# Kernel optimization log

Measured on AMD Instinct MI355X. Metric: run time of the kernel, lower is better.

## Reference

```python
import jax, jax.numpy as jnp
import numpy as np

B, C, H, W = 16, 64, 64, 64
K = 512  # n_embeddings


def setup_inputs() -> dict:
    key = jax.random.key(0)
    k1, k2 = jax.random.split(key)
    inputs = jax.random.normal(k1, (B, C, H, W), dtype=jnp.float32)
    emb_weight = jax.random.normal(k2, (K, C), dtype=jnp.float32)
    weight = jnp.ones((K,), dtype=jnp.float32)  # EMA cluster-size buffer
    return {"inputs": inputs, "emb_weight": emb_weight, "weight": weight}


def reference(inputs, emb_weight, weight):
    sg = jax.lax.stop_gradient
    # BCHW -> BHWC
    x = jnp.transpose(inputs, (0, 2, 3, 1))  # [B,H,W,C]
    flat = x.reshape(-1, x.shape[-1])        # [N,C]
    n = flat.shape[0]
    k = emb_weight.shape[0]
    # squared euclidean distances [N,K] (argmin identical to cdist argmin)
    d = (
        jnp.sum(flat * flat, axis=-1, keepdims=True)
        - 2.0 * (flat @ emb_weight.T)
        + jnp.sum(emb_weight * emb_weight, axis=-1)
    )
    indices = jnp.argmin(d, axis=1)  # [N]
    # avg_probs = mean over rows of one-hot mask == normalized histogram
    avg_probs = jnp.bincount(indices, length=k).astype(jnp.float32) / jnp.float32(n)
    perplexity = jnp.exp(-jnp.sum(avg_probs * jnp.log(avg_probs + 1e-10)))
    # straight-through quantization
    q = emb_weight[indices].reshape(x.shape)  # [B,H,W,C]
    quantized = sg(q) + x - sg(x)
    commitment_loss = jnp.mean((sg(quantized) - x) ** 2)
    active_codes = jnp.sum(weight >= 0.01)
    out = jnp.transpose(quantized, (0, 3, 1, 2))  # back to BCHW
    return out, commitment_loss, perplexity, active_codes, indices
```

## Files before the change

kernel.cpp:

```cpp
#include <hip/hip_runtime.h>

#define HW 4096
#define CHW 262144
#define OUT_ELEMS 4194304
#define FLT_BIG 3.4e38f

typedef __attribute__((ext_vector_type(8))) short  short8;
typedef __attribute__((ext_vector_type(4))) float  floatx4;
typedef __attribute__((ext_vector_type(4))) int    intx4;


__device__ __forceinline__ unsigned bf16_rne(float f) {
    unsigned u = __float_as_uint(f);
    return (u + 0x7FFFu + ((u >> 16) & 1u)) >> 16;
}

__device__ __forceinline__ void split8(const float* f, intx4* hi, intx4* lo) {
    unsigned h[4], l[4];
#pragma unroll
    for (int j = 0; j < 4; ++j) {
        const unsigned h0 = bf16_rne(f[2 * j]);
        const unsigned h1 = bf16_rne(f[2 * j + 1]);
        const float hf0 = __uint_as_float(h0 << 16);
        const float hf1 = __uint_as_float(h1 << 16);
        const unsigned l0 = bf16_rne(f[2 * j] - hf0);
        const unsigned l1 = bf16_rne(f[2 * j + 1] - hf1);
        h[j] = h0 | (h1 << 16);
        l[j] = l0 | (l1 << 16);
    }
    *hi = intx4{(int)h[0], (int)h[1], (int)h[2], (int)h[3]};
    *lo = intx4{(int)l[0], (int)l[1], (int)l[2], (int)l[3]};
}

__global__ void vq_prep(const float* __restrict__ emb,
                        unsigned short* __restrict__ pfrag,
                        float* __restrict__ enorm,
                        unsigned* __restrict__ hist,
                        unsigned* __restrict__ done) {
    const int t = threadIdx.x;
    const int lane = t & 63;
    if (blockIdx.x == 0) {
        hist[t] = 0u; hist[t + 256] = 0u;
        if (t == 0) *done = 0u;
    }
    const int code = (blockIdx.x << 2) + (t >> 6);
    const int c = lane;
    const float v = emb[(code << 6) + c];
    const unsigned hb = bf16_rne(v);
    const float hf    = __uint_as_float(hb << 16);
    const unsigned lb = bf16_rne(v - hf);
    const int nc = code >> 6, grp = (code & 63) >> 4, n = code & 15;
    const int q = (c & 31) >> 3, o = c & 7;
    const int jh = c >> 5;
    const int jl = 2 + (c >> 5);
    pfrag[((((size_t)(nc*4 + jh)*4 + grp)*4 + q)*16 + n)*8 + o] = (unsigned short)hb;
    pfrag[((((size_t)(nc*4 + jl)*4 + grp)*4 + q)*16 + n)*8 + o] = (unsigned short)lb;
    float s = v * v;
#pragma unroll
    for (int off = 32; off > 0; off >>= 1) s += __shfl_xor(s, off, 64);
    if (lane == 0) enorm[code] = -0.5f * s;
}

__global__ __launch_bounds__(256)
void vq_main(const float* __restrict__ x_in, const float* __restrict__ emb,
             const unsigned short* __restrict__ pfrag,
             const float* __restrict__ enorm,
             float* __restrict__ out, float* __restrict__ idx_out,
             double* __restrict__ ws_sse) {
    __shared__ unsigned short cbuf[2][8192];
    __shared__ float  b1s[2][64], b2s[2][64];
    __shared__ int    i1s[2][64], i2s[2][64];
    __shared__ int    c1i[64], c2i[64];
    __shared__ double parts[4][65];
    __shared__ double ls_red[4];

    const int t     = threadIdx.x;
    const int lane  = t & 63;
    const int wv    = t >> 6;
    const int col   = lane & 15;
    const int quad  = lane >> 4;
    const int blk   = blockIdx.x;
    const int khalf = wv & 1;
    const int mset  = wv >> 1;
    const int ncol0 = khalf << 5;
    const int b = blk >> 6, h = blk & 63;
    const float* xb = x_in + (size_t)b * CHW + h * 64;

    intx4 s0[4];
#pragma unroll
    for (int i = 0; i < 4; ++i)
        s0[i] = *(const intx4*)((const char*)pfrag + (i << 12) + (t << 4));

    short8 Xh[2][2], Xl[2][2];
#pragma unroll
    for (int T = 0; T < 2; ++T) {
        const int row = (mset << 5) + (T << 4) + col;
#pragma unroll
        for (int u = 0; u < 2; ++u) {
            float f[8];
#pragma unroll
            for (int j = 0; j < 8; ++j) {
                const int c = (u << 5) + (quad << 3) + j;
                f[j] = xb[(size_t)c * HW + row];
            }
            intx4 hi, lo;
            split8(f, &hi, &lo);
            Xh[T][u] = __builtin_bit_cast(short8, hi);
            Xl[T][u] = __builtin_bit_cast(short8, lo);
        }
    }

#pragma unroll
    for (int i = 0; i < 4; ++i)
        *(intx4*)((char*)&cbuf[0][0] + (i << 12) + (t << 4)) = s0[i];
    __syncthreads();

    float B1a[2], B2a[2], B1b[2], B2b[2];
    int   I1a[2], I2a[2], I1b[2], I2b[2];
#pragma unroll
    for (int T = 0; T < 2; ++T) {
        B1a[T] = -FLT_BIG; B2a[T] = -FLT_BIG; B1b[T] = -FLT_BIG; B2b[T] = -FLT_BIG;
        I1a[T] = 0x3FFFFFFF; I2a[T] = 0x3FFFFFFF; I1b[T] = 0x3FFFFFFF; I2b[T] = 0x3FFFFFFF;
    }

    const float* enp = enorm + ncol0 + (quad << 2);
    const int lbo = (khalf << 11) + (lane << 4);

#pragma unroll 2
    for (int nc = 0; nc < 8; ++nc) {
        const int cur = nc & 1;
        intx4 st[4];
        if (nc < 7) {
#pragma unroll
            for (int i = 0; i < 4; ++i)
                st[i] = *(const intx4*)((const char*)pfrag +
                          ((size_t)(nc + 1) << 14) + (i << 12) + (t << 4));
        }
        const int K0 = nc << 6;
        const floatx4 e0v = *(const floatx4*)(enp + K0);
        const floatx4 e1v = *(const floatx4*)(enp + K0 + 16);
        floatx4 a0[2] = {{0.f,0.f,0.f,0.f},{0.f,0.f,0.f,0.f}};
        floatx4 a1[2] = {{0.f,0.f,0.f,0.f},{0.f,0.f,0.f,0.f}};
        const char* base = (const char*)&cbuf[cur][0] + lbo;
#define BLD(j, g) (*(const short8*)(base + ((j) << 12) + ((g) << 10)))
        {
            const short8 e0 = BLD(0, 0), e1 = BLD(0, 1);
#pragma unroll
            for (int T = 0; T < 2; ++T) {
                a0[T] = __builtin_amdgcn_mfma_f32_16x16x32_bf16(e0, Xh[T][0], a0[T], 0, 0, 0);
                a1[T] = __builtin_amdgcn_mfma_f32_16x16x32_bf16(e1, Xh[T][0], a1[T], 0, 0, 0);
                a0[T] = __builtin_amdgcn_mfma_f32_16x16x32_bf16(e0, Xl[T][0], a0[T], 0, 0, 0);
                a1[T] = __builtin_amdgcn_mfma_f32_16x16x32_bf16(e1, Xl[T][0], a1[T], 0, 0, 0);
            }
        }
        {
            const short8 e0 = BLD(1, 0), e1 = BLD(1, 1);
#pragma unroll
            for (int T = 0; T < 2; ++T) {
                a0[T] = __builtin_amdgcn_mfma_f32_16x16x32_bf16(e0, Xh[T][1], a0[T], 0, 0, 0);
                a1[T] = __builtin_amdgcn_mfma_f32_16x16x32_bf16(e1, Xh[T][1], a1[T], 0, 0, 0);
                a0[T] = __builtin_amdgcn_mfma_f32_16x16x32_bf16(e0, Xl[T][1], a0[T], 0, 0, 0);
                a1[T] = __builtin_amdgcn_mfma_f32_16x16x32_bf16(e1, Xl[T][1], a1[T], 0, 0, 0);
            }
        }
        {
            const short8 e0 = BLD(2, 0), e1 = BLD(2, 1);
#pragma unroll
            for (int T = 0; T < 2; ++T) {
                a0[T] = __builtin_amdgcn_mfma_f32_16x16x32_bf16(e0, Xh[T][0], a0[T], 0, 0, 0);
                a1[T] = __builtin_amdgcn_mfma_f32_16x16x32_bf16(e1, Xh[T][0], a1[T], 0, 0, 0);
            }
        }
        {
            const short8 e0 = BLD(3, 0), e1 = BLD(3, 1);
#pragma unroll
            for (int T = 0; T < 2; ++T) {
                a0[T] = __builtin_amdgcn_mfma_f32_16x16x32_bf16(e0, Xh[T][1], a0[T], 0, 0, 0);
                a1[T] = __builtin_amdgcn_mfma_f32_16x16x32_bf16(e1, Xh[T][1], a1[T], 0, 0, 0);
            }
        }
#undef BLD

        const int cb = K0 + ncol0 + (quad << 2);
#pragma unroll
        for (int T = 0; T < 2; ++T) {
#pragma unroll
            for (int reg = 0; reg < 4; ++reg) {
                const float da = a0[T][reg] + e0v[reg];
                if (da > B1a[T])      { B2a[T] = B1a[T]; I2a[T] = I1a[T]; B1a[T] = da; I1a[T] = cb + reg; }
                else if (da > B2a[T]) { B2a[T] = da; I2a[T] = cb + reg; }
                const float db = a1[T][reg] + e1v[reg];
                if (db > B1b[T])      { B2b[T] = B1b[T]; I2b[T] = I1b[T]; B1b[T] = db; I1b[T] = cb + 16 + reg; }
                else if (db > B2b[T]) { B2b[T] = db; I2b[T] = cb + 16 + reg; }
            }
        }

        if (nc < 7) {
#pragma unroll
            for (int i = 0; i < 4; ++i)
                *(intx4*)((char*)&cbuf[cur ^ 1][0] + (i << 12) + (t << 4)) = st[i];
        }
        __syncthreads();
    }

#pragma unroll
    for (int T = 0; T < 2; ++T) {
        float B1, B2; int I1, I2;
        if (B1b[T] > B1a[T] || (B1b[T] == B1a[T] && I1b[T] < I1a[T])) {
            B1 = B1b[T]; I1 = I1b[T];
            if (B1a[T] > B2b[T] || (B1a[T] == B2b[T] && I1a[T] < I2b[T])) { B2 = B1a[T]; I2 = I1a[T]; }
            else                                                          { B2 = B2b[T]; I2 = I2b[T]; }
        } else {
            B1 = B1a[T]; I1 = I1a[T];
            if (B1b[T] > B2a[T] || (B1b[T] == B2a[T] && I1b[T] < I2a[T])) { B2 = B1b[T]; I2 = I1b[T]; }
            else                                                          { B2 = B2a[T]; I2 = I2a[T]; }
        }
#pragma unroll
        for (int off = 16; off <= 32; off <<= 1) {
            const float ob1 = __shfl_xor(B1, off, 64);
            const int   oi1 = __shfl_xor(I1, off, 64);
            const float ob2 = __shfl_xor(B2, off, 64);
            const int   oi2 = __shfl_xor(I2, off, 64);
            if (ob1 > B1 || (ob1 == B1 && oi1 < I1)) {
                float nb2; int ni2;
                if (B1 > ob2 || (B1 == ob2 && I1 < oi2)) { nb2 = B1; ni2 = I1; }
                else                                     { nb2 = ob2; ni2 = oi2; }
                B1 = ob1; I1 = oi1; B2 = nb2; I2 = ni2;
            } else if (ob1 > B2 || (ob1 == B2 && oi1 < I2)) {
                B2 = ob1; I2 = oi1;
            }
        }
        if (lane < 16) {
            const int row = (mset << 5) + (T << 4) + lane;
            b1s[khalf][row] = B1; b2s[khalf][row] = B2;
            i1s[khalf][row] = I1; i2s[khalf][row] = I2;
        }
    }
    __syncthreads();

    if (t < 64) {
        const int r = t;
        float b1 = b1s[0][r], b2 = b2s[0][r];
        int   i1 = i1s[0][r], i2 = i2s[0][r];
        const float c1 = b1s[1][r]; const int j1 = i1s[1][r];
        const float c2 = b2s[1][r]; const int j2 = i2s[1][r];
        if (c1 > b1 || (c1 == b1 && j1 < i1))      { b2 = b1; i2 = i1; b1 = c1; i1 = j1; }
        else if (c1 > b2 || (c1 == b2 && j1 < i2)) { b2 = c1; i2 = j1; }
        if (c2 > b2 || (c2 == b2 && j2 < i2))      { b2 = c2; i2 = j2; }
        c1i[r] = i1; c2i[r] = i2;
    }
    __syncthreads();

    const int r = t & 63;
    const int k = t >> 6;
    {
        const int ch = k >> 1;
        const int code = (k & 1) ? c2i[r] : c1i[r];
        const float* ep = emb + ((size_t)code << 6) + (ch << 5);
        const float* xq = xb + r;
        double d0 = 0.0, d1 = 0.0;
#pragma unroll
        for (int cc = 0; cc < 32; cc += 2) {
            const int c = (ch << 5) + cc;
            const double f0 = (double)xq[(size_t)c * HW]       - (double)ep[cc];
            const double f1 = (double)xq[(size_t)(c + 1) * HW] - (double)ep[cc + 1];
            d0 = fma(f0, f0, d0);
            d1 = fma(f1, f1, d1);
        }
        parts[k][r] = d0 + d1;
    }
    __syncthreads();

    int win;
    {
        const double d1 = parts[0][r] + parts[2][r];
        const double d2 = parts[1][r] + parts[3][r];
        win = c1i[r];
        const int i2 = c2i[r];
        if (d2 < d1 || (d2 == d1 && i2 < win)) win = i2;
        if (t < 64) idx_out[(blk << 6) + r] = (float)win;
    }

    {
        const int c0 = k << 4;
        const float* xp = xb + r;
        float*       op = out + (size_t)b * CHW + h * 64 + r;
        const float* eq = emb + ((size_t)win << 6);
        float sse_local = 0.f;
#pragma unroll
        for (int cc = 0; cc < 16; ++cc) {
            const int c = c0 + cc;
            const float qc = eq[c];
            const float dx = qc - xp[(size_t)c * HW];
            sse_local = fmaf(dx, dx, sse_local);
            op[(size_t)c * HW] = qc;
        }
#pragma unroll
        for (int off = 32; off > 0; off >>= 1)
            sse_local += __shfl_down(sse_local, off, 64);
        if (lane == 0) ls_red[wv] = (double)sse_local;
        __syncthreads();
        if (t == 0)
            ws_sse[blk] = (ls_red[0] + ls_red[1]) + (ls_red[2] + ls_red[3]);
    }
}

__global__ void vq_hist2(const float* __restrict__ idx_out,
                         const double* __restrict__ ws_sse,
                         const float* __restrict__ weight,
                         unsigned* __restrict__ hist,
                         unsigned* __restrict__ done,
                         float* __restrict__ scal) {
    __shared__ unsigned hs[512];
    __shared__ double redt[4], reds[4];
    __shared__ int    redi[4], lastf;
    const int t = threadIdx.x;
    const int lane = t & 63, wv = t >> 6;
    hs[t] = 0u; hs[t + 256] = 0u;
    __syncthreads();
    const float4* ip = (const float4*)(idx_out + (blockIdx.x << 12));
#pragma unroll
    for (int i = 0; i < 4; ++i) {
        const float4 v = ip[(i << 8) + t];
        atomicAdd(&hs[(int)v.x], 1u);
        atomicAdd(&hs[(int)v.y], 1u);
        atomicAdd(&hs[(int)v.z], 1u);
        atomicAdd(&hs[(int)v.w], 1u);
    }
    __syncthreads();
    if (hs[t])       atomicAdd(&hist[t],       hs[t]);
    if (hs[t + 256]) atomicAdd(&hist[t + 256], hs[t + 256]);
    __syncthreads();

    if (t == 0) {
        lastf = (__hip_atomic_fetch_add(done, 1u, __ATOMIC_RELAXED,
                                        __HIP_MEMORY_SCOPE_AGENT) == 15u) ? 1 : 0;
    }
    __syncthreads();
    if (lastf) {
        double term = 0.0, ssep = 0.0; int act = 0;
#pragma unroll
        for (int j = 0; j < 2; ++j) {
            const int kk = t + (j << 8);
            const unsigned cnt =
                __hip_atomic_load(&hist[kk], __ATOMIC_RELAXED, __HIP_MEMORY_SCOPE_AGENT);
            const double pr = (double)cnt * (1.0 / 65536.0);
            term += pr * log(pr + 1e-10);
            act  += (weight[kk] >= 0.01f) ? 1 : 0;
        }
#pragma unroll
        for (int j = 0; j < 4; ++j) ssep += ws_sse[t + (j << 8)];
#pragma unroll
        for (int off = 32; off > 0; off >>= 1) {
            term += __shfl_down(term, off, 64);
            ssep += __shfl_down(ssep, off, 64);
            act  += __shfl_down(act,  off, 64);
        }
        if (lane == 0) { redt[wv] = term; reds[wv] = ssep; redi[wv] = act; }
        __syncthreads();
        if (t == 0) {
            const double s  = (redt[0] + redt[1]) + (redt[2] + redt[3]);
            const double ss = (reds[0] + reds[1]) + (reds[2] + reds[3]);
            const int    a  = redi[0] + redi[1] + redi[2] + redi[3];
            scal[0] = (float)(ss * (1.0 / 4194304.0));
            scal[1] = (float)exp(-s);
            scal[2] = (float)a;
        }
    }
}

extern "C" void kernel_launch(void* const* d_in, const int* in_sizes, int n_in,
                              void* d_out, int out_size, void* d_ws, size_t ws_size,
                              hipStream_t stream) {
    const float* x      = (const float*)d_in[0];
    const float* emb    = (const float*)d_in[1];
    const float* weight = (const float*)d_in[2];

    float* out = (float*)d_out;
    float*          enorm  = (float*)d_ws;
    unsigned short* pfrag  = (unsigned short*)((char*)d_ws + 4096);
    double*         ws_sse = (double*)((char*)d_ws + 135168);
    unsigned*       hist   = (unsigned*)((char*)d_ws + 143360);
    unsigned*       done   = (unsigned*)((char*)d_ws + 145408);

    float* scal    = out + OUT_ELEMS;
    float* idx_out = out + OUT_ELEMS + 3;

    vq_prep<<<128, 256, 0, stream>>>(emb, pfrag, enorm, hist, done);
    vq_main<<<1024, 256, 0, stream>>>(x, emb, pfrag, enorm, out, idx_out, ws_sse);
    vq_hist2<<<16, 256, 0, stream>>>(idx_out, ws_sse, weight, hist, done, scal);
}
```

Before: 102.6 us.

## Fuse codebook bf16 split into main kernel and drop prep launch

Removes the separate prep kernel. Each main-kernel block now loads raw fp32 codebook chunks, splits them into hi/lo bf16 fragments and computes the code norms into shared memory inside the double-buffered loop. The histogram kernel no longer uses a zeroed global histogram and counter; each block writes its own partial histogram and raises a magic-value flag, and blocks that see all flags set do the final reduction. This saves a launch and the global zeroing, at the cost of redundant codebook conversion in every block. The flags are never reset, so on later calls a block can see stale flags and reduce stale partials. That is a correctness risk.

```diff
diff --git a/kernel.cpp b/kernel.cpp
--- a/kernel.cpp
+++ b/kernel.cpp
@@ -32,42 +32,24 @@
     *lo = intx4{(int)l[0], (int)l[1], (int)l[2], (int)l[3]};
 }
 
-__global__ void vq_prep(const float* __restrict__ emb,
-                        unsigned short* __restrict__ pfrag,
-                        float* __restrict__ enorm,
-                        unsigned* __restrict__ hist,
-                        unsigned* __restrict__ done) {
-    const int t = threadIdx.x;
-    const int lane = t & 63;
-    if (blockIdx.x == 0) {
-        hist[t] = 0u; hist[t + 256] = 0u;
-        if (t == 0) *done = 0u;
-    }
-    const int code = (blockIdx.x << 2) + (t >> 6);
-    const int c = lane;
-    const float v = emb[(code << 6) + c];
-    const unsigned hb = bf16_rne(v);
-    const float hf    = __uint_as_float(hb << 16);
-    const unsigned lb = bf16_rne(v - hf);
-    const int nc = code >> 6, grp = (code & 63) >> 4, n = code & 15;
-    const int q = (c & 31) >> 3, o = c & 7;
-    const int jh = c >> 5;
-    const int jl = 2 + (c >> 5);
-    pfrag[((((size_t)(nc*4 + jh)*4 + grp)*4 + q)*16 + n)*8 + o] = (unsigned short)hb;
-    pfrag[((((size_t)(nc*4 + jl)*4 + grp)*4 + q)*16 + n)*8 + o] = (unsigned short)lb;
-    float s = v * v;
-#pragma unroll
-    for (int off = 32; off > 0; off >>= 1) s += __shfl_xor(s, off, 64);
-    if (lane == 0) enorm[code] = -0.5f * s;
+__device__ __forceinline__ void split4(float v0, float v1, float v2, float v3,
+                                       int2* hi, int2* lo) {
+    const unsigned h0 = bf16_rne(v0), h1 = bf16_rne(v1);
+    const unsigned h2 = bf16_rne(v2), h3 = bf16_rne(v3);
+    const unsigned l0 = bf16_rne(v0 - __uint_as_float(h0 << 16));
+    const unsigned l1 = bf16_rne(v1 - __uint_as_float(h1 << 16));
+    const unsigned l2 = bf16_rne(v2 - __uint_as_float(h2 << 16));
+    const unsigned l3 = bf16_rne(v3 - __uint_as_float(h3 << 16));
+    *hi = int2{(int)(h0 | (h1 << 16)), (int)(h2 | (h3 << 16))};
+    *lo = int2{(int)(l0 | (l1 << 16)), (int)(l2 | (l3 << 16))};
 }
 
 __global__ __launch_bounds__(256)
 void vq_main(const float* __restrict__ x_in, const float* __restrict__ emb,
-             const unsigned short* __restrict__ pfrag,
-             const float* __restrict__ enorm,
              float* __restrict__ out, float* __restrict__ idx_out,
              double* __restrict__ ws_sse) {
-    __shared__ unsigned short cbuf[2][8192];
+    __shared__ __align__(16) unsigned short cbuf[2][8192];
+    __shared__ __align__(16) float enorm_s[2][64];
     __shared__ float  b1s[2][64], b2s[2][64];
     __shared__ int    i1s[2][64], i2s[2][64];
     __shared__ int    c1i[64], c2i[64];
@@ -86,10 +68,13 @@
     const int b = blk >> 6, h = blk & 63;
     const float* xb = x_in + (size_t)b * CHW + h * 64;
 
-    intx4 s0[4];
+    const int cvt_off = ((t & 15) >> 3) * 4096 + (((t & 15) >> 1) & 3) * 256
+                      + (t >> 4) * 16 + ((t & 15) & 1) * 8;
+
+    float4 s0[4];
 #pragma unroll
     for (int i = 0; i < 4; ++i)
-        s0[i] = *(const intx4*)((const char*)pfrag + (i << 12) + (t << 4));
+        s0[i] = *(const float4*)(emb + (i << 10) + (t << 2));
 
     short8 Xh[2][2], Xl[2][2];
 #pragma unroll
@@ -110,9 +95,29 @@
         }
     }
 
-#pragma unroll
-    for (int i = 0; i < 4; ++i)
-        *(intx4*)((char*)&cbuf[0][0] + (i << 12) + (t << 4)) = s0[i];
+    {
+        char* cbn = (char*)&cbuf[0][0];
+        float ss[4];
+#pragma unroll
+        for (int i = 0; i < 4; ++i) {
+            const float4 v = s0[i];
+            int2 hi, lo;
+            split4(v.x, v.y, v.z, v.w, &hi, &lo);
+            *(int2*)(cbn + cvt_off + (i << 10))        = hi;
+            *(int2*)(cbn + cvt_off + (i << 10) + 8192) = lo;
+            ss[i] = fmaf(v.x, v.x, fmaf(v.y, v.y, fmaf(v.z, v.z, v.w * v.w)));
+        }
+#pragma unroll
+        for (int off = 1; off <= 8; off <<= 1) {
+#pragma unroll
+            for (int i = 0; i < 4; ++i) ss[i] += __shfl_xor(ss[i], off, 64);
+        }
+        if ((lane & 15) == 0) {
+#pragma unroll
+            for (int i = 0; i < 4; ++i)
+                enorm_s[0][(i << 4) + (t >> 4)] = -0.5f * ss[i];
+        }
+    }
     __syncthreads();
 
     float B1a[2], B2a[2], B1b[2], B2b[2];
@@ -123,22 +128,20 @@
         I1a[T] = 0x3FFFFFFF; I2a[T] = 0x3FFFFFFF; I1b[T] = 0x3FFFFFFF; I2b[T] = 0x3FFFFFFF;
     }
 
-    const float* enp = enorm + ncol0 + (quad << 2);
     const int lbo = (khalf << 11) + (lane << 4);
 
 #pragma unroll 2
     for (int nc = 0; nc < 8; ++nc) {
         const int cur = nc & 1;
-        intx4 st[4];
+        float4 st[4];
         if (nc < 7) {
 #pragma unroll
             for (int i = 0; i < 4; ++i)
-                st[i] = *(const intx4*)((const char*)pfrag +
-                          ((size_t)(nc + 1) << 14) + (i << 12) + (t << 4));
+                st[i] = *(const float4*)(emb + ((nc + 1) << 12) + (i << 10) + (t << 2));
         }
         const int K0 = nc << 6;
-        const floatx4 e0v = *(const floatx4*)(enp + K0);
-        const floatx4 e1v = *(const floatx4*)(enp + K0 + 16);
+        const floatx4 e0v = *(const floatx4*)&enorm_s[cur][ncol0 + (quad << 2)];
+        const floatx4 e1v = *(const floatx4*)&enorm_s[cur][ncol0 + (quad << 2) + 16];
         floatx4 a0[2] = {{0.f,0.f,0.f,0.f},{0.f,0.f,0.f,0.f}};
         floatx4 a1[2] = {{0.f,0.f,0.f,0.f},{0.f,0.f,0.f,0.f}};
         const char* base = (const char*)&cbuf[cur][0] + lbo;
@@ -196,9 +199,27 @@
         }
 
         if (nc < 7) {
-#pragma unroll
-            for (int i = 0; i < 4; ++i)
-                *(intx4*)((char*)&cbuf[cur ^ 1][0] + (i << 12) + (t << 4)) = st[i];
+            char* cbn = (char*)&cbuf[cur ^ 1][0];
+            float ss[4];
+#pragma unroll
+            for (int i = 0; i < 4; ++i) {
+                const float4 v = st[i];
+                int2 hi, lo;
+                split4(v.x, v.y, v.z, v.w, &hi, &lo);
+                *(int2*)(cbn + cvt_off + (i << 10))        = hi;
+                *(int2*)(cbn + cvt_off + (i << 10) + 8192) = lo;
+                ss[i] = fmaf(v.x, v.x, fmaf(v.y, v.y, fmaf(v.z, v.z, v.w * v.w)));
+            }
+#pragma unroll
+            for (int off = 1; off <= 8; off <<= 1) {
+#pragma unroll
+                for (int i = 0; i < 4; ++i) ss[i] += __shfl_xor(ss[i], off, 64);
+            }
+            if ((lane & 15) == 0) {
+#pragma unroll
+                for (int i = 0; i < 4; ++i)
+                    enorm_s[cur ^ 1][(i << 4) + (t >> 4)] = -0.5f * ss[i];
+            }
         }
         __syncthreads();
     }
@@ -308,17 +329,18 @@
 __global__ void vq_hist2(const float* __restrict__ idx_out,
                          const double* __restrict__ ws_sse,
                          const float* __restrict__ weight,
-                         unsigned* __restrict__ hist,
-                         unsigned* __restrict__ done,
+                         unsigned* __restrict__ part,
+                         unsigned* __restrict__ flags,
                          float* __restrict__ scal) {
     __shared__ unsigned hs[512];
     __shared__ double redt[4], reds[4];
     __shared__ int    redi[4], lastf;
     const int t = threadIdx.x;
+    const int blk = blockIdx.x;
     const int lane = t & 63, wv = t >> 6;
     hs[t] = 0u; hs[t + 256] = 0u;
     __syncthreads();
-    const float4* ip = (const float4*)(idx_out + (blockIdx.x << 12));
+    const float4* ip = (const float4*)(idx_out + (blk << 12));
 #pragma unroll
     for (int i = 0; i < 4; ++i) {
         const float4 v = ip[(i << 8) + t];
@@ -328,13 +350,22 @@
         atomicAdd(&hs[(int)v.w], 1u);
     }
     __syncthreads();
-    if (hs[t])       atomicAdd(&hist[t],       hs[t]);
-    if (hs[t + 256]) atomicAdd(&hist[t + 256], hs[t + 256]);
-    __syncthreads();
-
+    __hip_atomic_store(&part[(blk << 9) + t],       hs[t],
+                       __ATOMIC_RELAXED, __HIP_MEMORY_SCOPE_AGENT);
+    __hip_atomic_store(&part[(blk << 9) + t + 256], hs[t + 256],
+                       __ATOMIC_RELAXED, __HIP_MEMORY_SCOPE_AGENT);
+    __syncthreads();
     if (t == 0) {
-        lastf = (__hip_atomic_fetch_add(done, 1u, __ATOMIC_RELAXED,
-                                        __HIP_MEMORY_SCOPE_AGENT) == 15u) ? 1 : 0;
+        __hip_atomic_store(&flags[blk], 0x51C0FFEEu ^ (unsigned)blk,
+                           __ATOMIC_RELAXED, __HIP_MEMORY_SCOPE_AGENT);
+        asm volatile("s_waitcnt vmcnt(0)" ::: "memory");
+        int all = 1;
+#pragma unroll
+        for (int p = 0; p < 16; ++p)
+            all &= (__hip_atomic_load(&flags[p], __ATOMIC_RELAXED,
+                                      __HIP_MEMORY_SCOPE_AGENT)
+                    == (0x51C0FFEEu ^ (unsigned)p)) ? 1 : 0;
+        lastf = all;
     }
     __syncthreads();
     if (lastf) {
@@ -342,8 +373,11 @@
 #pragma unroll
         for (int j = 0; j < 2; ++j) {
             const int kk = t + (j << 8);
-            const unsigned cnt =
-                __hip_atomic_load(&hist[kk], __ATOMIC_RELAXED, __HIP_MEMORY_SCOPE_AGENT);
+            unsigned cnt = 0;
+#pragma unroll
+            for (int p = 0; p < 16; ++p)
+                cnt += __hip_atomic_load(&part[(p << 9) + kk], __ATOMIC_RELAXED,
+                                         __HIP_MEMORY_SCOPE_AGENT);
             const double pr = (double)cnt * (1.0 / 65536.0);
             term += pr * log(pr + 1e-10);
             act  += (weight[kk] >= 0.01f) ? 1 : 0;
@@ -377,16 +411,13 @@
     const float* weight = (const float*)d_in[2];
 
     float* out = (float*)d_out;
-    float*          enorm  = (float*)d_ws;
-    unsigned short* pfrag  = (unsigned short*)((char*)d_ws + 4096);
-    double*         ws_sse = (double*)((char*)d_ws + 135168);
-    unsigned*       hist   = (unsigned*)((char*)d_ws + 143360);
-    unsigned*       done   = (unsigned*)((char*)d_ws + 145408);
+    double*   ws_sse = (double*)d_ws;
+    unsigned* part   = (unsigned*)((char*)d_ws + 8192);
+    unsigned* flags  = (unsigned*)((char*)d_ws + 40960);
 
     float* scal    = out + OUT_ELEMS;
     float* idx_out = out + OUT_ELEMS + 3;
 
-    vq_prep<<<128, 256, 0, stream>>>(emb, pfrag, enorm, hist, done);
-    vq_main<<<1024, 256, 0, stream>>>(x, emb, pfrag, enorm, out, idx_out, ws_sse);
-    vq_hist2<<<16, 256, 0, stream>>>(idx_out, ws_sse, weight, hist, done, scal);
-}
+    vq_main<<<1024, 256, 0, stream>>>(x, emb, out, idx_out, ws_sse);
+    vq_hist2<<<16, 256, 0, stream>>>(idx_out, ws_sse, weight, part, flags, scal);
+}
```

Measured after the change: 120.3 us. 1.17x slower.
